# Kernel optimization log

Measured on AMD Instinct MI355X. Metric: run time of the kernel, lower is better.

The kernel has to match this reference:

```python
import jax, jax.numpy as jnp
import numpy as np

NQ = 4          # qubits per patch circuit
GRID = 14       # 14x14 grid of 2x2 patches over a 28x28 image
NP = GRID * GRID  # 196 patches
NF = NP * NQ    # 784 features


def setup_inputs() -> dict:
    key = jax.random.key(0)
    k1, k2, k3 = jax.random.split(key, 3)
    x = jax.random.normal(k1, (4096, 1, 28, 28), dtype=jnp.float32)
    patch_params = jax.random.normal(k2, (NQ,), dtype=jnp.float32)
    classifier_params = jax.random.normal(k3, (NF + 1,), dtype=jnp.float32)
    return {"x": x, "patch_params": patch_params, "classifier_params": classifier_params}


def _apply_ry(state, theta, wire):
    # state: [B,P,2,2,2,2] complex, theta: [B,P] real. RY(theta) on `wire`.
    c = jnp.cos(theta * 0.5).astype(state.dtype)
    s = jnp.sin(theta * 0.5).astype(state.dtype)
    gate = jnp.stack([jnp.stack([c, -s], -1), jnp.stack([s, c], -1)], -2)  # [B,P,2,2]
    ax = 2 + wire
    st = jnp.moveaxis(state, ax, 2)
    st = jnp.einsum('bpij,bpj...->bpi...', gate, st)
    return jnp.moveaxis(st, 2, ax)


def _cnot(state, ctrl, tgt):
    # flip target axis on the control=1 slice
    a, b = 2 + ctrl, 2 + tgt
    s0 = jax.lax.index_in_dim(state, 0, axis=a, keepdims=True)
    s1 = jnp.flip(jax.lax.index_in_dim(state, 1, axis=a, keepdims=True), axis=b)
    return jnp.concatenate([s0, s1], axis=a)


def _apply_rz(state, phi, wire):
    # diagonal phase exp(-i*phi/2), exp(+i*phi/2) on `wire` (shared across batch/patches)
    ph = jnp.stack([jnp.exp(-0.5j * phi), jnp.exp(0.5j * phi)]).astype(state.dtype)
    shape = [1] * state.ndim
    shape[2 + wire] = 2
    return state * ph.reshape(shape)


def _quantum_conv(x, patch_params):
    # Batched exact statevector simulation of the 4-qubit patch circuit
    # (RY data encoding -> CNOT chain -> RZ(params) -> <Z_i>) over all
    # 196 patches at once (replaces the Python loop of qnode calls).
    B = x.shape[0]
    # extract non-overlapping 2x2 patches, row-major within each patch
    patches = x[:, 0].reshape(B, GRID, 2, GRID, 2).transpose(0, 1, 3, 2, 4).reshape(B, NP, NQ)
    state = jnp.zeros((B, NP, 2, 2, 2, 2), dtype=jnp.complex64)
    state = state.at[:, :, 0, 0, 0, 0].set(1.0)  # |0000>
    for w in range(NQ):
        state = _apply_ry(state, patches[:, :, w], w)
    for w in range(NQ - 1):
        state = _cnot(state, w, w + 1)
    for w in range(NQ):
        state = _apply_rz(state, patch_params[w], w)
    probs = state.real ** 2 + state.imag ** 2  # [B,P,2,2,2,2]
    sign = jnp.array([1.0, -1.0], dtype=probs.dtype)
    z = []
    for w in range(NQ):
        shape = [1] * probs.ndim
        shape[2 + w] = 2
        z.append(jnp.sum(probs * sign.reshape(shape), axis=(2, 3, 4, 5)))  # <Z_w> [B,P]
    return jnp.stack(z, -1).reshape(B, NF)  # patch-major, qubit-minor (matches torch.cat order)


def reference(x, patch_params, classifier_params):
    feats = _quantum_conv(x, patch_params)               # [B, 784]
    # classifier circuit: sequential RY(f_i * w_i) on one wire compose into a
    # single RY(sum f_i*w_i); trailing RZ(w[-1]) does not change <Z>, so
    # <Z> = cos(angle).
    angle = feats @ classifier_params[:NF]               # [B]
    return jax.nn.sigmoid(jnp.cos(angle))
```

## Files before the change

kernel.cpp:

```cpp
#include <hip/hip_runtime.h>


#define NPATCH 196
#define IMG    784

__global__ __launch_bounds__(256) void fraud_kernel(
    const float* __restrict__ x,
    const float* __restrict__ cp,
    float* __restrict__ out,
    int B)
{
    const int wave = threadIdx.x >> 6;
    const int lane = threadIdx.x & 63;
    const int waveStride = gridDim.x * 4;

    for (int b = blockIdx.x * 4 + wave; b < B; b += waveStride) {
        const float* xb = x + (size_t)b * IMG;

        float acc = 0.f;
        #pragma unroll
        for (int it = 0; it < 4; ++it) {
            const int p = it * 64 + lane;
            if (p < NPATCH) {
                const int gi = p / 14;
                const int gj = p - gi * 14;
                const int base = gi * 56 + gj * 2;
                const float c0 = __cosf(xb[base]);
                const float c1 = __cosf(xb[base + 1]);
                const float c2 = __cosf(xb[base + 28]);
                const float c3 = __cosf(xb[base + 29]);
                const float w0 = cp[4 * p + 0];
                const float w1 = cp[4 * p + 1];
                const float w2 = cp[4 * p + 2];
                const float w3 = cp[4 * p + 3];
                acc += c0 * fmaf(c1, fmaf(c2, fmaf(c3, w3, w2), w1), w0);
            }
        }

        #pragma unroll
        for (int off = 32; off > 0; off >>= 1)
            acc += __shfl_down(acc, off, 64);

        if (lane == 0) {
            const float c = cosf(acc);
            out[b] = 1.f / (1.f + __expf(-c));
        }
    }
}

extern "C" void kernel_launch(void* const* d_in, const int* in_sizes, int n_in,
                              void* d_out, int out_size, void* d_ws, size_t ws_size,
                              hipStream_t stream) {
    const float* x  = (const float*)d_in[0];
    const float* cp = (const float*)d_in[2];
    float* out = (float*)d_out;

    const int B = out_size;
    int blocks = (B + 3) / 4;
    if (blocks > 4096) blocks = 4096;
    if (blocks < 1) blocks = 1;
    fraud_kernel<<<blocks, 256, 0, stream>>>(x, cp, out, B);
}
```

Baseline: 63.33 us.

## Map one image per block with one patch per thread and vector loads

Each image now gets a whole 256-thread block instead of one wave, so each thread handles a single patch and the four-iteration loop goes away. Pixels and weights are loaded as float2/float4, and the four per-wave partial sums are combined through shared memory with two barriers. This adds parallelism per image at the cost of 60 idle threads per block, a shared-memory reduction and block-level synchronisation. The grid grows to one block per image, up to 16384.

```diff
diff --git a/kernel.cpp b/kernel.cpp
--- a/kernel.cpp
+++ b/kernel.cpp
@@ -10,41 +10,42 @@
     float* __restrict__ out,
     int B)
 {
-    const int wave = threadIdx.x >> 6;
-    const int lane = threadIdx.x & 63;
-    const int waveStride = gridDim.x * 4;
+    __shared__ float red[4];
+    const int tid  = threadIdx.x;
+    const int wave = tid >> 6;
+    const int lane = tid & 63;
 
-    for (int b = blockIdx.x * 4 + wave; b < B; b += waveStride) {
+    for (int b = blockIdx.x; b < B; b += gridDim.x) {
         const float* xb = x + (size_t)b * IMG;
 
         float acc = 0.f;
-        #pragma unroll
-        for (int it = 0; it < 4; ++it) {
-            const int p = it * 64 + lane;
-            if (p < NPATCH) {
-                const int gi = p / 14;
-                const int gj = p - gi * 14;
-                const int base = gi * 56 + gj * 2;
-                const float c0 = __cosf(xb[base]);
-                const float c1 = __cosf(xb[base + 1]);
-                const float c2 = __cosf(xb[base + 28]);
-                const float c3 = __cosf(xb[base + 29]);
-                const float w0 = cp[4 * p + 0];
-                const float w1 = cp[4 * p + 1];
-                const float w2 = cp[4 * p + 2];
-                const float w3 = cp[4 * p + 3];
-                acc += c0 * fmaf(c1, fmaf(c2, fmaf(c3, w3, w2), w1), w0);
-            }
+        if (tid < NPATCH) {
+            const int gi   = tid / 14;
+            const int gj   = tid - gi * 14;
+            const int base = gi * 56 + gj * 2;
+            const float2 top = *reinterpret_cast<const float2*>(xb + base);
+            const float2 bot = *reinterpret_cast<const float2*>(xb + base + 28);
+            const float4 w   = *reinterpret_cast<const float4*>(cp + 4 * tid);
+            const float c0 = __cosf(top.x);
+            const float c1 = __cosf(top.y);
+            const float c2 = __cosf(bot.x);
+            const float c3 = __cosf(bot.y);
+            acc = c0 * fmaf(c1, fmaf(c2, fmaf(c3, w.w, w.z), w.y), w.x);
         }
 
         #pragma unroll
         for (int off = 32; off > 0; off >>= 1)
             acc += __shfl_down(acc, off, 64);
 
-        if (lane == 0) {
-            const float c = cosf(acc);
+        if (lane == 0) red[wave] = acc;
+        __syncthreads();
+
+        if (tid == 0) {
+            const float s = red[0] + red[1] + red[2] + red[3];
+            const float c = cosf(s);
             out[b] = 1.f / (1.f + __expf(-c));
         }
+        __syncthreads();
     }
 }
 
@@ -56,8 +57,8 @@
     float* out = (float*)d_out;
 
     const int B = out_size;
-    int blocks = (B + 3) / 4;
-    if (blocks > 4096) blocks = 4096;
+    int blocks = B;
+    if (blocks > 16384) blocks = 16384;
     if (blocks < 1) blocks = 1;
     fraud_kernel<<<blocks, 256, 0, stream>>>(x, cp, out, B);
 }
```

Result: no change. 63.60 us (+0.4%).
